# Kernel tuning notes

Hardware: AMD Instinct MI355X
Metric: run time of the kernel (lower is better)

Reference implementation:

```python
import jax, jax.numpy as jnp
import numpy as np
from jax import lax

B, C, H, W = 32, 1, 224, 224
OUT, K, STRIDE, PAD = 64, 5, 1, 2
D = C * K * K

def _make_weight(key):
    # torch kaiming_uniform_(a=0, fan_in=D, gain=sqrt(2)): bound = sqrt(6/fan_in)
    bound = np.sqrt(6.0 / D)
    w = jax.random.uniform(key, (OUT, D), jnp.float32, -bound, bound)
    w = w.at[0].set(-1.0)
    w = w.at[1].set(1.0)
    return w

def setup_inputs() -> dict:
    key = jax.random.key(0)
    kx, kw = jax.random.split(key)
    x = jax.random.normal(kx, (B, C, H, W), jnp.float32)
    weight = _make_weight(kw)
    return {"x": x, "weight": weight}

def reference(x, weight):
    # im2col: [B, C*K*K, H', W']  (channel-major patch ordering matches torch unfold for C=1)
    patches = lax.conv_general_dilated_patches(
        x, (K, K), (STRIDE, STRIDE), [(PAD, PAD), (PAD, PAD)])
    b, d, hp, wp = patches.shape
    win = patches.reshape(b, d, hp * wp).transpose(0, 2, 1)  # [B, L, D]
    x2 = jnp.sum(win * win, axis=-1, keepdims=True)          # [B, L, 1]
    w2 = jnp.sum(weight * weight, axis=-1)                   # [O]
    xw = jnp.einsum('bld,od->blo', win, weight)              # [B, L, O]
    d2 = jnp.maximum(x2 + w2[None, None, :] - 2.0 * xw, 0.0)
    dist = jnp.sqrt(d2)                                      # [B, L, O]
    return dist.transpose(0, 2, 1).reshape(b, OUT, hp, wp)
```

## Files before the change

kernel.cpp:

```cpp
#include <hip/hip_runtime.h>

#define BB    32
#define HH    224
#define WW    224
#define OUTC  64
#define KK    5
#define PADP  2
#define LL    (HH * WW)

__global__ __launch_bounds__(256) void gray_conv_kernel(
    const float* __restrict__ x,
    const float* __restrict__ wgt,
    float* __restrict__ out)
{
    __shared__ float sw[OUTC][28];
    __shared__ float sw2[OUTC];

    const int tid = threadIdx.x;

    for (int i = tid; i < OUTC * 25; i += 256) {
        sw[i / 25][i % 25] = wgt[i];
    }
    __syncthreads();
    if (tid < OUTC) {
        float s = 0.f;
        #pragma unroll
        for (int d = 0; d < 25; ++d) { float v = sw[tid][d]; s = fmaf(v, v, s); }
        sw2[tid] = s;
    }
    __syncthreads();

    const int pos = blockIdx.x * 256 + tid;
    const int b   = pos / LL;
    const int rem = pos - b * LL;
    const int h   = rem / WW;
    const int w   = rem - h * WW;

    const float* xb = x + (size_t)b * LL;

    float p[25];
    float x2 = 0.f;
    #pragma unroll
    for (int ky = 0; ky < KK; ++ky) {
        const int  yy  = h + ky - PADP;
        const int  yc  = min(max(yy, 0), HH - 1);
        const bool oky = (unsigned)yy < (unsigned)HH;
        #pragma unroll
        for (int kx = 0; kx < KK; ++kx) {
            const int  xx = w + kx - PADP;
            const int  xc = min(max(xx, 0), WW - 1);
            const bool ok = oky && ((unsigned)xx < (unsigned)WW);
            float v = xb[yc * WW + xc];
            v = ok ? v : 0.f;
            p[ky * KK + kx] = v;
            x2 = fmaf(v, v, x2);
        }
    }

    float* ob = out + (size_t)b * OUTC * LL + rem;
    #pragma unroll 4
    for (int o = 0; o < OUTC; ++o) {
        float dot = 0.f;
        #pragma unroll
        for (int d = 0; d < 25; ++d) dot = fmaf(p[d], sw[o][d], dot);
        float d2 = fmaf(-2.f, dot, x2 + sw2[o]);
        d2 = fmaxf(d2, 0.f);
        ob[(size_t)o * LL] = sqrtf(d2);
    }
}

extern "C" void kernel_launch(void* const* d_in, const int* in_sizes, int n_in,
                              void* d_out, int out_size, void* d_ws, size_t ws_size,
                              hipStream_t stream) {
    const float* x   = (const float*)d_in[0];
    const float* wgt = (const float*)d_in[1];
    float* out       = (float*)d_out;

    const int total  = BB * LL;
    const int blocks = total / 256;
    gray_conv_kernel<<<dim3(blocks), dim3(256), 0, stream>>>(x, wgt, out);
}
```

Before: 474.4 us.

## Compute four adjacent output pixels per thread with shared patch rows and float4 stores

Each thread now handles four horizontally adjacent positions. It loads a 5x8 input window once and reuses it across the overlapping 5x5 patches. This amortizes the shared-memory weight reads over four positions and writes outputs as float4 vectors, which reduces load and store instruction counts. In exchange it uses more registers and launches a quarter as many blocks, which may reduce occupancy. The kernel is likely bound by output writes (about 411 MB).

```diff
diff --git a/kernel.cpp b/kernel.cpp
--- a/kernel.cpp
+++ b/kernel.cpp
@@ -7,6 +7,7 @@
 #define KK    5
 #define PADP  2
 #define LL    (HH * WW)
+#define TPOS  4
 
 __global__ __launch_bounds__(256) void gray_conv_kernel(
     const float* __restrict__ x,
@@ -30,42 +31,69 @@
     }
     __syncthreads();
 
-    const int pos = blockIdx.x * 256 + tid;
-    const int b   = pos / LL;
-    const int rem = pos - b * LL;
-    const int h   = rem / WW;
-    const int w   = rem - h * WW;
+    const int pos0 = (blockIdx.x * 256 + tid) * TPOS;
+    const int b    = pos0 / LL;
+    const int rem  = pos0 - b * LL;
+    const int h    = rem / WW;
+    const int w0   = rem - h * WW;
 
     const float* xb = x + (size_t)b * LL;
 
-    float p[25];
-    float x2 = 0.f;
+    float pr[KK][KK + TPOS - 1];
     #pragma unroll
     for (int ky = 0; ky < KK; ++ky) {
         const int  yy  = h + ky - PADP;
         const int  yc  = min(max(yy, 0), HH - 1);
         const bool oky = (unsigned)yy < (unsigned)HH;
+        const float* xr = xb + yc * WW;
         #pragma unroll
-        for (int kx = 0; kx < KK; ++kx) {
-            const int  xx = w + kx - PADP;
-            const int  xc = min(max(xx, 0), WW - 1);
-            const bool ok = oky && ((unsigned)xx < (unsigned)WW);
-            float v = xb[yc * WW + xc];
-            v = ok ? v : 0.f;
-            p[ky * KK + kx] = v;
-            x2 = fmaf(v, v, x2);
+        for (int c = 0; c < KK + TPOS - 1; ++c) {
+            const int  xxi = w0 + c - PADP;
+            const int  xc  = min(max(xxi, 0), WW - 1);
+            const bool ok  = oky && ((unsigned)xxi < (unsigned)WW);
+            float v = xr[xc];
+            pr[ky][c] = ok ? v : 0.f;
         }
     }
 
+    float x2[TPOS];
+    #pragma unroll
+    for (int j = 0; j < TPOS; ++j) {
+        float s = 0.f;
+        #pragma unroll
+        for (int ky = 0; ky < KK; ++ky)
+            #pragma unroll
+            for (int kx = 0; kx < KK; ++kx) {
+                float v = pr[ky][j + kx];
+                s = fmaf(v, v, s);
+            }
+        x2[j] = s;
+    }
+
     float* ob = out + (size_t)b * OUTC * LL + rem;
-    #pragma unroll 4
+    #pragma unroll 2
     for (int o = 0; o < OUTC; ++o) {
-        float dot = 0.f;
+        float dot[TPOS] = {0.f, 0.f, 0.f, 0.f};
         #pragma unroll
-        for (int d = 0; d < 25; ++d) dot = fmaf(p[d], sw[o][d], dot);
-        float d2 = fmaf(-2.f, dot, x2 + sw2[o]);
-        d2 = fmaxf(d2, 0.f);
-        ob[(size_t)o * LL] = sqrtf(d2);
+        for (int ky = 0; ky < KK; ++ky) {
+            #pragma unroll
+            for (int kx = 0; kx < KK; ++kx) {
+                const float wv = sw[o][ky * KK + kx];
+                #pragma unroll
+                for (int j = 0; j < TPOS; ++j)
+                    dot[j] = fmaf(pr[ky][j + kx], wv, dot[j]);
+            }
+        }
+        const float w2 = sw2[o];
+        float4 r;
+        {
+            float d2;
+            d2 = fmaxf(fmaf(-2.f, dot[0], x2[0] + w2), 0.f); r.x = sqrtf(d2);
+            d2 = fmaxf(fmaf(-2.f, dot[1], x2[1] + w2), 0.f); r.y = sqrtf(d2);
+            d2 = fmaxf(fmaf(-2.f, dot[2], x2[2] + w2), 0.f); r.z = sqrtf(d2);
+            d2 = fmaxf(fmaf(-2.f, dot[3], x2[3] + w2), 0.f); r.w = sqrtf(d2);
+        }
+        *(float4*)(ob + (size_t)o * LL) = r;
     }
 }
 
@@ -77,6 +105,6 @@
     float* out       = (float*)d_out;
 
     const int total  = BB * LL;
-    const int blocks = total / 256;
+    const int blocks = total / (256 * TPOS);
     gray_conv_kernel<<<dim3(blocks), dim3(256), 0, stream>>>(x, wgt, out);
 }
```

Result: slower. 491.4 us (+3.6%).
